# Kernel tuning notes

Hardware: AMD Instinct MI355X
Metric: run time of the kernel (lower is better)

Reference implementation:

```python
import jax, jax.numpy as jnp
import numpy as np

N = 100000
E = 1600000
F_IN, H, C = 128, 128, 64


def setup_inputs() -> dict:
    key = jax.random.key(0)
    ks = jax.random.split(key, 8)
    x = jax.random.normal(ks[0], (N, F_IN), dtype=jnp.float32)
    edge_index = jax.random.randint(ks[1], (2, E), 0, N, dtype=jnp.int64)
    s = lambda fi: (1.0 / np.sqrt(fi))
    # SAGEConv1: lin_l (applied to mean-aggregated neighbors, has bias), lin_r (root, no bias)
    W1l = jax.random.uniform(ks[2], (H, F_IN), jnp.float32, -s(F_IN), s(F_IN))
    b1 = jnp.zeros((H,), jnp.float32)
    W1r = jax.random.uniform(ks[3], (H, F_IN), jnp.float32, -s(F_IN), s(F_IN))
    # SAGEConv2
    W2l = jax.random.uniform(ks[4], (C, H), jnp.float32, -s(H), s(H))
    b2 = jnp.zeros((C,), jnp.float32)
    W2r = jax.random.uniform(ks[5], (C, H), jnp.float32, -s(H), s(H))
    return {"x": x, "edge_index": edge_index, "W1l": W1l, "b1": b1, "W1r": W1r,
            "W2l": W2l, "b2": b2, "W2r": W2r}


def _mean_aggr(x, src, dst):
    # mean over incoming neighbors (PyG flow: edge_index[0]=source -> edge_index[1]=target)
    msg = x[src]                                            # [E, F] big gather
    summed = jax.ops.segment_sum(msg, dst, num_segments=N)  # [N, F]
    cnt = jax.ops.segment_sum(jnp.ones((src.shape[0],), x.dtype), dst, num_segments=N)
    return summed / jnp.clip(cnt, 1.0)[:, None]


def _sage_conv(x, src, dst, Wl, b, Wr):
    agg = _mean_aggr(x, src, dst)
    return agg @ Wl.T + b + x @ Wr.T


def _iconv(x, src, dst):
    # weight-free GCN propagation: D^-1/2 (A + I) D^-1/2 @ x
    loops = jnp.arange(N, dtype=src.dtype)
    s2 = jnp.concatenate([src, loops])
    d2 = jnp.concatenate([dst, loops])
    deg = jax.ops.segment_sum(jnp.ones((s2.shape[0],), x.dtype), d2, num_segments=N)
    dis = jnp.where(deg > 0, jax.lax.rsqrt(jnp.maximum(deg, 1.0)), 0.0)
    norm = dis[s2] * dis[d2]                               # [E+N]
    return jax.ops.segment_sum(norm[:, None] * x[s2], d2, num_segments=N)


def reference(x, edge_index, W1l, b1, W1r, W2l, b2, W2r):
    src, dst = edge_index[0], edge_index[1]
    h = jax.nn.relu(_sage_conv(x, src, dst, W1l, b1, W1r))
    # F.dropout(training=False) -> identity in eval mode
    h = _sage_conv(h, src, dst, W2l, b2, W2r)
    return _iconv(h, src, dst)
```

## Files before the change

### kernel.cpp

```cpp
#include <hip/hip_runtime.h>

#define GN 100000
#define GE 1600000
#define GF 128
#define GH 128
#define GC 64

#define NB 392
#define SLABSZ 5376
#define P1_EDGES 4096

typedef __attribute__((ext_vector_type(8))) short v8s;
typedef __attribute__((ext_vector_type(4))) float v4f;

__device__ __forceinline__ unsigned short f2bf(float f) {
    union { float f; unsigned u; } a; a.f = f;
    unsigned r = a.u + 0x7fff + ((a.u >> 16) & 1);
    return (unsigned short)(r >> 16);
}
__device__ __forceinline__ float bf2f(unsigned short b) {
    union { unsigned u; float f; } a; a.u = ((unsigned)b) << 16;
    return a.f;
}

__global__ __launch_bounds__(256) void bucket_pass1_kernel(
    unsigned* __restrict__ slab, int* __restrict__ bucket_cnt,
    const int* __restrict__ src, const int* __restrict__ dst, int E)
{
    __shared__ int hist[512];
    __shared__ int scanex[512];
    __shared__ int cursor[512];
    __shared__ int gbase[512];
    __shared__ int ssum[256];
    __shared__ unsigned stage[P1_EDGES];
    __shared__ unsigned short sbid[P1_EDGES];

    int tid = threadIdx.x;
    int e0 = blockIdx.x * P1_EDGES;
    int nE = min(P1_EDGES, E - e0);

    unsigned pk[16]; int bk[16];
    hist[tid] = 0; hist[tid + 256] = 0;
    __syncthreads();
    #pragma unroll
    for (int j = 0; j < 16; ++j) {
        int i = j * 256 + tid;
        if (i < nE) {
            int e = e0 + i;
            int d = dst[e], s = src[e];
            int b = d >> 8;
            pk[j] = ((unsigned)(d & 255) << 17) | (unsigned)s;
            bk[j] = b;
            atomicAdd(&hist[b], 1);
        } else bk[j] = -1;
    }
    __syncthreads();
    int a0 = hist[2 * tid], a1 = hist[2 * tid + 1];
    int s2 = a0 + a1;
    ssum[tid] = s2;
    __syncthreads();
    for (int off = 1; off < 256; off <<= 1) {
        int v = (tid >= off) ? ssum[tid - off] : 0;
        __syncthreads();
        ssum[tid] += v;
        __syncthreads();
    }
    int pbase = ssum[tid] - s2;
    scanex[2 * tid] = pbase;          cursor[2 * tid] = pbase;
    scanex[2 * tid + 1] = pbase + a0; cursor[2 * tid + 1] = pbase + a0;
    __syncthreads();
    #pragma unroll
    for (int j = 0; j < 16; ++j) {
        if (bk[j] >= 0) {
            int pos = atomicAdd(&cursor[bk[j]], 1);
            stage[pos] = pk[j];
            sbid[pos] = (unsigned short)bk[j];
        }
    }
    for (int b = tid; b < NB; b += 256) {
        int c = hist[b];
        gbase[b] = c ? atomicAdd(&bucket_cnt[b], c) : 0;
    }
    __syncthreads();
    for (int i = tid; i < nE; i += 256) {
        int b = sbid[i];
        int go = gbase[b] + (i - scanex[b]);
        if (go < SLABSZ)
            slab[(size_t)b * SLABSZ + go] = stage[i];
    }
}

__global__ void bucket_scan_kernel(const int* __restrict__ bucket_cnt,
                                   int* __restrict__ bucket_start,
                                   int* __restrict__ row_ptr, int E) {
    __shared__ int ssum[256];
    int t = threadIdx.x;
    int c0 = (2 * t < NB) ? bucket_cnt[2 * t] : 0;
    int c1 = (2 * t + 1 < NB) ? bucket_cnt[2 * t + 1] : 0;
    int s = c0 + c1;
    ssum[t] = s;
    __syncthreads();
    for (int off = 1; off < 256; off <<= 1) {
        int v = (t >= off) ? ssum[t - off] : 0;
        __syncthreads();
        ssum[t] += v;
        __syncthreads();
    }
    int pbase = ssum[t] - s;
    if (2 * t < NB) bucket_start[2 * t] = pbase;
    if (2 * t + 1 < NB) bucket_start[2 * t + 1] = pbase + c0;
    if (t == 0) row_ptr[GN] = E;
}

__global__ __launch_bounds__(256) void bucket_pass2_kernel(
    int* __restrict__ csr, int* __restrict__ row_ptr,
    float* __restrict__ invc, float* __restrict__ dis,
    const unsigned* __restrict__ slab, const int* __restrict__ bucket_cnt,
    const int* __restrict__ bucket_start)
{
    __shared__ int deg_l[256];
    __shared__ int excl[256];
    __shared__ int cur[256];
    __shared__ int ssum[256];
    __shared__ unsigned stage[SLABSZ];

    int t = threadIdx.x;
    int b = blockIdx.x;
    int cnt = min(bucket_cnt[b], SLABSZ);
    int base = bucket_start[b];
    const unsigned* sp = slab + (size_t)b * SLABSZ;

    deg_l[t] = 0;
    __syncthreads();
    for (int i = t; i < cnt; i += 256)
        atomicAdd(&deg_l[sp[i] >> 17], 1);
    __syncthreads();
    int dg = deg_l[t];
    ssum[t] = dg;
    __syncthreads();
    for (int off = 1; off < 256; off <<= 1) {
        int v = (t >= off) ? ssum[t - off] : 0;
        __syncthreads();
        ssum[t] += v;
        __syncthreads();
    }
    int ex = ssum[t] - dg;
    excl[t] = ex; cur[t] = ex;
    __syncthreads();
    int d = b * 256 + t;
    if (d < GN) {
        row_ptr[d] = base + ex;
        float c = (float)dg;
        invc[d] = 1.0f / fmaxf(c, 1.0f);
        dis[d] = rsqrtf(c + 1.0f);
    }
    for (int i = t; i < cnt; i += 256) {
        unsigned p = sp[i];
        int pos = atomicAdd(&cur[p >> 17], 1);
        stage[pos] = p & 0x1FFFFu;
    }
    __syncthreads();
    for (int i = t; i < cnt; i += 256)
        csr[base + i] = (int)stage[i];
}

__global__ void cast_all_kernel(unsigned short* __restrict__ xb, const float* __restrict__ x,
                                unsigned short* w1l, unsigned short* w1r,
                                unsigned short* w2l, unsigned short* w2r,
                                const float* W1l, const float* W1r,
                                const float* W2l, const float* W2r) {
    int blk = blockIdx.x;
    if (blk < 12500) {
        int i = blk * 256 + threadIdx.x;
        float4 v = ((const float4*)x)[i];
        ushort4 u;
        u.x = f2bf(v.x); u.y = f2bf(v.y); u.z = f2bf(v.z); u.w = f2bf(v.w);
        ((ushort4*)xb)[i] = u;
        return;
    }
    int i = (blk - 12500) * 256 + threadIdx.x;
    const float* s; unsigned short* d; int off;
    if      (i <  4096) { s = W1l; d = w1l; off = i; }
    else if (i <  8192) { s = W1r; d = w1r; off = i - 4096; }
    else if (i < 10240) { s = W2l; d = w2l; off = i - 8192; }
    else if (i < 12288) { s = W2r; d = w2r; off = i - 10240; }
    else return;
    float4 v = ((const float4*)s)[off];
    ushort4 u;
    u.x = f2bf(v.x); u.y = f2bf(v.y); u.z = f2bf(v.z); u.w = f2bf(v.w);
    ((ushort4*)d)[off] = u;
}

__global__ __launch_bounds__(256) void dual_gemm_kernel(
    unsigned short* __restrict__ C,
    const unsigned short* __restrict__ A1, const unsigned short* __restrict__ A2,
    const unsigned short* __restrict__ W1, const unsigned short* __restrict__ W2,
    const float* __restrict__ bias, int M)
{
    int tid = threadIdx.x;
    int wv = tid >> 6, lane = tid & 63;
    int lm = lane & 15, quad = lane >> 4;
    int m_base = blockIdx.x * 256 + wv * 64;
    int n_base = blockIdx.y * 64;

    v4f acc[4][4];
    #pragma unroll
    for (int mt = 0; mt < 4; ++mt)
        #pragma unroll
        for (int nt = 0; nt < 4; ++nt) acc[mt][nt] = (v4f){0.f,0.f,0.f,0.f};

    #pragma unroll
    for (int ks = 0; ks < 4; ++ks) {
        int koff = ks * 32 + quad * 8;
        v8s a1[4], a2[4], b1[4], b2[4];
        #pragma unroll
        for (int mt = 0; mt < 4; ++mt) {
            int row = m_base + mt * 16 + lm;
            if (row < M) {
                a1[mt] = *(const v8s*)(A1 + (size_t)row * 128 + koff);
                a2[mt] = *(const v8s*)(A2 + (size_t)row * 128 + koff);
            } else {
                a1[mt] = (v8s){0,0,0,0,0,0,0,0};
                a2[mt] = (v8s){0,0,0,0,0,0,0,0};
            }
        }
        #pragma unroll
        for (int nt = 0; nt < 4; ++nt) {
            int col = n_base + nt * 16 + lm;
            b1[nt] = *(const v8s*)(W1 + (size_t)col * 128 + koff);
            b2[nt] = *(const v8s*)(W2 + (size_t)col * 128 + koff);
        }
        #pragma unroll
        for (int mt = 0; mt < 4; ++mt)
            #pragma unroll
            for (int nt = 0; nt < 4; ++nt) {
                acc[mt][nt] = __builtin_amdgcn_mfma_f32_16x16x32_bf16(a1[mt], b1[nt], acc[mt][nt], 0, 0, 0);
                acc[mt][nt] = __builtin_amdgcn_mfma_f32_16x16x32_bf16(a2[mt], b2[nt], acc[mt][nt], 0, 0, 0);
            }
    }

    #pragma unroll
    for (int mt = 0; mt < 4; ++mt)
        #pragma unroll
        for (int r = 0; r < 4; ++r) {
            int row = m_base + mt * 16 + quad * 4 + r;
            if (row >= M) continue;
            #pragma unroll
            for (int nt = 0; nt < 4; ++nt) {
                int col = n_base + nt * 16 + lm;
                float v = acc[mt][nt][r] + bias[col];
                v = fmaxf(v, 0.f);
                C[(size_t)row * 128 + col] = f2bf(v);
            }
        }
}

__global__ __launch_bounds__(256) void gemm64_dual_kernel(
    unsigned short* __restrict__ P, unsigned short* __restrict__ Q,
    const unsigned short* __restrict__ A,
    const unsigned short* __restrict__ Wl, const unsigned short* __restrict__ Wr,
    const float* __restrict__ b2, int M)
{
    int tid = threadIdx.x;
    int wv = tid >> 6, lane = tid & 63;
    int lm = lane & 15, quad = lane >> 4;
    int m_base = blockIdx.x * 256 + wv * 64;

    v4f accP[4][4], accQ[4][4];
    #pragma unroll
    for (int mt = 0; mt < 4; ++mt)
        #pragma unroll
        for (int nt = 0; nt < 4; ++nt) {
            accP[mt][nt] = (v4f){0.f,0.f,0.f,0.f};
            accQ[mt][nt] = (v4f){0.f,0.f,0.f,0.f};
        }

    #pragma unroll
    for (int ks = 0; ks < 4; ++ks) {
        int koff = ks * 32 + quad * 8;
        v8s af[4], bl[4], br[4];
        #pragma unroll
        for (int mt = 0; mt < 4; ++mt) {
            int row = m_base + mt * 16 + lm;
            if (row < M) af[mt] = *(const v8s*)(A + (size_t)row * 128 + koff);
            else         af[mt] = (v8s){0,0,0,0,0,0,0,0};
        }
        #pragma unroll
        for (int nt = 0; nt < 4; ++nt) {
            int col = nt * 16 + lm;
            bl[nt] = *(const v8s*)(Wl + (size_t)col * 128 + koff);
            br[nt] = *(const v8s*)(Wr + (size_t)col * 128 + koff);
        }
        #pragma unroll
        for (int mt = 0; mt < 4; ++mt)
            #pragma unroll
            for (int nt = 0; nt < 4; ++nt) {
                accP[mt][nt] = __builtin_amdgcn_mfma_f32_16x16x32_bf16(af[mt], bl[nt], accP[mt][nt], 0, 0, 0);
                accQ[mt][nt] = __builtin_amdgcn_mfma_f32_16x16x32_bf16(af[mt], br[nt], accQ[mt][nt], 0, 0, 0);
            }
    }

    #pragma unroll
    for (int mt = 0; mt < 4; ++mt)
        #pragma unroll
        for (int r = 0; r < 4; ++r) {
            int row = m_base + mt * 16 + quad * 4 + r;
            if (row >= M) continue;
            #pragma unroll
            for (int nt = 0; nt < 4; ++nt) {
                int col = nt * 16 + lm;
                P[(size_t)row * 64 + col] = f2bf(accP[mt][nt][r]);
                Q[(size_t)row * 64 + col] = f2bf(accQ[mt][nt][r] + b2[col]);
            }
        }
}

__global__ __launch_bounds__(256) void gather_mean128_kernel(
    unsigned short* __restrict__ out, const unsigned short* __restrict__ in,
    const float* __restrict__ invc, const int* __restrict__ row_ptr,
    const int* __restrict__ csr, int N)
{
    int wid = (blockIdx.x * 256 + threadIdx.x) >> 6;
    int lane = threadIdx.x & 63;
    if (wid >= N) return;
    int half = lane >> 5, k = lane & 31;
    int beg = row_ptr[wid], end = row_ptr[wid + 1];
    float ax = 0.f, ay = 0.f, az = 0.f, aw = 0.f;
    int j = beg + half;
    for (; j + 6 < end; j += 8) {
        int s0 = csr[j], s1 = csr[j + 2], s2 = csr[j + 4], s3 = csr[j + 6];
        ushort4 a = ((const ushort4*)(in + (size_t)s0 * 128))[k];
        ushort4 b = ((const ushort4*)(in + (size_t)s1 * 128))[k];
        ushort4 c = ((const ushort4*)(in + (size_t)s2 * 128))[k];
        ushort4 d = ((const ushort4*)(in + (size_t)s3 * 128))[k];
        ax += (bf2f(a.x) + bf2f(b.x)) + (bf2f(c.x) + bf2f(d.x));
        ay += (bf2f(a.y) + bf2f(b.y)) + (bf2f(c.y) + bf2f(d.y));
        az += (bf2f(a.z) + bf2f(b.z)) + (bf2f(c.z) + bf2f(d.z));
        aw += (bf2f(a.w) + bf2f(b.w)) + (bf2f(c.w) + bf2f(d.w));
    }
    for (; j < end; j += 2) {
        ushort4 a = ((const ushort4*)(in + (size_t)csr[j] * 128))[k];
        ax += bf2f(a.x); ay += bf2f(a.y); az += bf2f(a.z); aw += bf2f(a.w);
    }
    ax += __shfl_xor(ax, 32); ay += __shfl_xor(ay, 32);
    az += __shfl_xor(az, 32); aw += __shfl_xor(aw, 32);
    if (half == 0) {
        float ic = invc[wid];
        ushort4 o;
        o.x = f2bf(ax * ic); o.y = f2bf(ay * ic);
        o.z = f2bf(az * ic); o.w = f2bf(aw * ic);
        ((ushort4*)(out + (size_t)wid * 128))[k] = o;
    }
}

__global__ __launch_bounds__(256) void gather_combine_kernel(
    unsigned short* __restrict__ h2s, const unsigned short* __restrict__ p,
    const unsigned short* __restrict__ q,
    const float* __restrict__ invc, const float* __restrict__ dis,
    const int* __restrict__ row_ptr, const int* __restrict__ csr, int N)
{
    int wid = (blockIdx.x * 256 + threadIdx.x) >> 6;
    int lane = threadIdx.x & 63;
    if (wid >= N) return;
    int half = lane >> 5, k = lane & 31;
    int beg = row_ptr[wid], end = row_ptr[wid + 1];
    float ax = 0.f, ay = 0.f;
    int j = beg + half;
    for (; j + 6 < end; j += 8) {
        int s0 = csr[j], s1 = csr[j + 2], s2 = csr[j + 4], s3 = csr[j + 6];
        unsigned a = ((const unsigned*)(p + (size_t)s0 * 64))[k];
        unsigned b = ((const unsigned*)(p + (size_t)s1 * 64))[k];
        unsigned c = ((const unsigned*)(p + (size_t)s2 * 64))[k];
        unsigned d = ((const unsigned*)(p + (size_t)s3 * 64))[k];
        ax += (bf2f((unsigned short)(a & 0xffff)) + bf2f((unsigned short)(b & 0xffff)))
            + (bf2f((unsigned short)(c & 0xffff)) + bf2f((unsigned short)(d & 0xffff)));
        ay += (bf2f((unsigned short)(a >> 16)) + bf2f((unsigned short)(b >> 16)))
            + (bf2f((unsigned short)(c >> 16)) + bf2f((unsigned short)(d >> 16)));
    }
    for (; j < end; j += 2) {
        unsigned a = ((const unsigned*)(p + (size_t)csr[j] * 64))[k];
        ax += bf2f((unsigned short)(a & 0xffff));
        ay += bf2f((unsigned short)(a >> 16));
    }
    ax += __shfl_xor(ax, 32); ay += __shfl_xor(ay, 32);
    if (half == 0) {
        float ic = invc[wid], dd = dis[wid];
        unsigned qv = ((const unsigned*)(q + (size_t)wid * 64))[k];
        float ox = dd * (ax * ic + bf2f((unsigned short)(qv & 0xffff)));
        float oy = dd * (ay * ic + bf2f((unsigned short)(qv >> 16)));
        unsigned o = (unsigned)f2bf(ox) | ((unsigned)f2bf(oy) << 16);
        ((unsigned*)(h2s + (size_t)wid * 64))[k] = o;
    }
}

__global__ __launch_bounds__(256) void iconv_kernel(
    float* __restrict__ out, const unsigned short* __restrict__ h2s,
    const float* __restrict__ dis, const int* __restrict__ row_ptr,
    const int* __restrict__ csr, int N)
{
    int wid = (blockIdx.x * 256 + threadIdx.x) >> 6;
    int lane = threadIdx.x & 63;
    if (wid >= N) return;
    int half = lane >> 5, k = lane & 31;
    int beg = row_ptr[wid], end = row_ptr[wid + 1];
    float ax = 0.f, ay = 0.f;
    int j = beg + half;
    for (; j + 6 < end; j += 8) {
        int s0 = csr[j], s1 = csr[j + 2], s2 = csr[j + 4], s3 = csr[j + 6];
        unsigned a = ((const unsigned*)(h2s + (size_t)s0 * 64))[k];
        unsigned b = ((const unsigned*)(h2s + (size_t)s1 * 64))[k];
        unsigned c = ((const unsigned*)(h2s + (size_t)s2 * 64))[k];
        unsigned d = ((const unsigned*)(h2s + (size_t)s3 * 64))[k];
        ax += (bf2f((unsigned short)(a & 0xffff)) + bf2f((unsigned short)(b & 0xffff)))
            + (bf2f((unsigned short)(c & 0xffff)) + bf2f((unsigned short)(d & 0xffff)));
        ay += (bf2f((unsigned short)(a >> 16)) + bf2f((unsigned short)(b >> 16)))
            + (bf2f((unsigned short)(c >> 16)) + bf2f((unsigned short)(d >> 16)));
    }
    for (; j < end; j += 2) {
        unsigned a = ((const unsigned*)(h2s + (size_t)csr[j] * 64))[k];
        ax += bf2f((unsigned short)(a & 0xffff));
        ay += bf2f((unsigned short)(a >> 16));
    }
    ax += __shfl_xor(ax, 32); ay += __shfl_xor(ay, 32);
    if (half == 0) {
        unsigned s = ((const unsigned*)(h2s + (size_t)wid * 64))[k];
        ax += bf2f((unsigned short)(s & 0xffff));
        ay += bf2f((unsigned short)(s >> 16));
        float dd = dis[wid];
        ((float2*)(out + (size_t)wid * 64))[k] = make_float2(dd * ax, dd * ay);
    }
}

extern "C" void kernel_launch(void* const* d_in, const int* in_sizes, int n_in,
                              void* d_out, int out_size, void* d_ws, size_t ws_size,
                              hipStream_t stream) {
    const float* x   = (const float*)d_in[0];
    const int*   ei  = (const int*)d_in[1];
    const float* W1l = (const float*)d_in[2];
    const float* b1  = (const float*)d_in[3];
    const float* W1r = (const float*)d_in[4];
    const float* W2l = (const float*)d_in[5];
    const float* b2  = (const float*)d_in[6];
    const float* W2r = (const float*)d_in[7];
    float* out = (float*)d_out;

    const int* src = ei;
    const int* dst = ei + GE;

    float* invc = (float*)d_ws;
    float* dis  = invc + GN;
    unsigned short* regA = (unsigned short*)(dis + GN);
    unsigned short* regB = regA + (size_t)GN * 128;
    unsigned short* regC = regB + (size_t)GN * 128;
    unsigned short* xb    = regA;
    unsigned short* aggx  = regB;
    unsigned short* hb    = regC;
    unsigned short* pb    = regA;
    unsigned short* qb    = regA + (size_t)GN * 64;
    unsigned short* h2s   = regB;
    unsigned short* w1lb = regC + (size_t)GN * 128;
    unsigned short* w1rb = w1lb + GH * GF;
    unsigned short* w2lb = w1rb + GH * GF;
    unsigned short* w2rb = w2lb + GC * GH;
    int* row_ptr      = (int*)(w2rb + GC * GH);
    int* bucket_cnt   = row_ptr + GN + 1;
    int* bucket_start = bucket_cnt + NB;
    unsigned* slab    = (unsigned*)(bucket_start + NB);
    int* csr          = (int*)(slab + (size_t)NB * SLABSZ);

    const int T = 256;
    const int g_wave = (GN * 64 + T - 1) / T;
    dim3 g_dual((GN + 255) / 256, GH / 64);
    dim3 g_g64((GN + 255) / 256, 1);

    hipMemsetAsync(bucket_cnt, 0, NB * sizeof(int), stream);
    bucket_pass1_kernel<<<(GE + P1_EDGES - 1) / P1_EDGES, T, 0, stream>>>(
        slab, bucket_cnt, src, dst, GE);
    bucket_scan_kernel<<<1, T, 0, stream>>>(bucket_cnt, bucket_start, row_ptr, GE);
    bucket_pass2_kernel<<<NB, T, 0, stream>>>(csr, row_ptr, invc, dis,
                                              slab, bucket_cnt, bucket_start);

    cast_all_kernel<<<12548, T, 0, stream>>>(xb, x, w1lb, w1rb, w2lb, w2rb,
                                             W1l, W1r, W2l, W2r);

    gather_mean128_kernel<<<g_wave, T, 0, stream>>>(aggx, xb, invc, row_ptr, csr, GN);
    dual_gemm_kernel<<<g_dual, T, 0, stream>>>(hb, aggx, xb, w1lb, w1rb, b1, GN);

    gemm64_dual_kernel<<<g_g64, T, 0, stream>>>(pb, qb, hb, w2lb, w2rb, b2, GN);
    gather_combine_kernel<<<g_wave, T, 0, stream>>>(h2s, pb, qb, invc, dis,
                                                    row_ptr, csr, GN);

    iconv_kernel<<<g_wave, T, 0, stream>>>(out, h2s, dis, row_ptr, csr, GN);
}
```

Measured before the change: 396.5 us.

## Fuse bucket pass1 with casts, fold bucket scan into pass2, loop N-halves in GEMM

```diff
diff --git a/kernel.cpp b/kernel.cpp
--- a/kernel.cpp
+++ b/kernel.cpp
@@ -9,6 +9,8 @@
 #define NB 392
 #define SLABSZ 5376
 #define P1_EDGES 4096
+#define P1_BLOCKS ((GE + P1_EDGES - 1) / P1_EDGES)
+#define CASTX_BLOCKS 12500
 
 typedef __attribute__((ext_vector_type(8))) short v8s;
 typedef __attribute__((ext_vector_type(4))) float v4f;
@@ -23,9 +25,14 @@
     return a.f;
 }
 
-__global__ __launch_bounds__(256) void bucket_pass1_kernel(
+__global__ __launch_bounds__(256) void prep_kernel(
     unsigned* __restrict__ slab, int* __restrict__ bucket_cnt,
-    const int* __restrict__ src, const int* __restrict__ dst, int E)
+    const int* __restrict__ src, const int* __restrict__ dst,
+    unsigned short* __restrict__ xb, const float* __restrict__ x,
+    unsigned short* w1l, unsigned short* w1r,
+    unsigned short* w2l, unsigned short* w2r,
+    const float* W1l, const float* W1r,
+    const float* W2l, const float* W2r)
 {
     __shared__ int hist[512];
     __shared__ int scanex[512];
@@ -36,8 +43,34 @@
     __shared__ unsigned short sbid[P1_EDGES];
 
     int tid = threadIdx.x;
-    int e0 = blockIdx.x * P1_EDGES;
-    int nE = min(P1_EDGES, E - e0);
+    int blk = blockIdx.x;
+
+    if (blk >= P1_BLOCKS) {
+        int cb = blk - P1_BLOCKS;
+        if (cb < CASTX_BLOCKS) {
+            int i = cb * 256 + tid;
+            float4 v = ((const float4*)x)[i];
+            ushort4 u;
+            u.x = f2bf(v.x); u.y = f2bf(v.y); u.z = f2bf(v.z); u.w = f2bf(v.w);
+            ((ushort4*)xb)[i] = u;
+            return;
+        }
+        int i = (cb - CASTX_BLOCKS) * 256 + tid;
+        const float* s; unsigned short* d; int off;
+        if      (i <  4096) { s = W1l; d = w1l; off = i; }
+        else if (i <  8192) { s = W1r; d = w1r; off = i - 4096; }
+        else if (i < 10240) { s = W2l; d = w2l; off = i - 8192; }
+        else if (i < 12288) { s = W2r; d = w2r; off = i - 10240; }
+        else return;
+        float4 v = ((const float4*)s)[off];
+        ushort4 u;
+        u.x = f2bf(v.x); u.y = f2bf(v.y); u.z = f2bf(v.z); u.w = f2bf(v.w);
+        ((ushort4*)d)[off] = u;
+        return;
+    }
+
+    int e0 = blk * P1_EDGES;
+    int nE = min(P1_EDGES, GE - e0);
 
     unsigned pk[16]; int bk[16];
     hist[tid] = 0; hist[tid + 256] = 0;
@@ -90,48 +123,42 @@
     }
 }
 
-__global__ void bucket_scan_kernel(const int* __restrict__ bucket_cnt,
-                                   int* __restrict__ bucket_start,
-                                   int* __restrict__ row_ptr, int E) {
-    __shared__ int ssum[256];
-    int t = threadIdx.x;
-    int c0 = (2 * t < NB) ? bucket_cnt[2 * t] : 0;
-    int c1 = (2 * t + 1 < NB) ? bucket_cnt[2 * t + 1] : 0;
-    int s = c0 + c1;
-    ssum[t] = s;
-    __syncthreads();
-    for (int off = 1; off < 256; off <<= 1) {
-        int v = (t >= off) ? ssum[t - off] : 0;
-        __syncthreads();
-        ssum[t] += v;
-        __syncthreads();
-    }
-    int pbase = ssum[t] - s;
-    if (2 * t < NB) bucket_start[2 * t] = pbase;
-    if (2 * t + 1 < NB) bucket_start[2 * t + 1] = pbase + c0;
-    if (t == 0) row_ptr[GN] = E;
-}
-
 __global__ __launch_bounds__(256) void bucket_pass2_kernel(
     int* __restrict__ csr, int* __restrict__ row_ptr,
     float* __restrict__ invc, float* __restrict__ dis,
-    const unsigned* __restrict__ slab, const int* __restrict__ bucket_cnt,
-    const int* __restrict__ bucket_start)
+    const unsigned* __restrict__ slab, const int* __restrict__ bucket_cnt)
 {
     __shared__ int deg_l[256];
     __shared__ int excl[256];
     __shared__ int cur[256];
     __shared__ int ssum[256];
+    __shared__ int bstart_s;
     __shared__ unsigned stage[SLABSZ];
 
     int t = threadIdx.x;
     int b = blockIdx.x;
+
+    int c0 = (2 * t < NB) ? bucket_cnt[2 * t] : 0;
+    int c1 = (2 * t + 1 < NB) ? bucket_cnt[2 * t + 1] : 0;
+    int sc = c0 + c1;
+    ssum[t] = sc;
+    __syncthreads();
+    for (int off = 1; off < 256; off <<= 1) {
+        int v = (t >= off) ? ssum[t - off] : 0;
+        __syncthreads();
+        ssum[t] += v;
+        __syncthreads();
+    }
+    int pb = ssum[t] - sc;
+    if (2 * t == b)     bstart_s = pb;
+    if (2 * t + 1 == b) bstart_s = pb + c0;
+    if (b == NB - 1 && t == 0) row_ptr[GN] = GE;
+
     int cnt = min(bucket_cnt[b], SLABSZ);
-    int base = bucket_start[b];
     const unsigned* sp = slab + (size_t)b * SLABSZ;
-
     deg_l[t] = 0;
     __syncthreads();
+    int base = bstart_s;
     for (int i = t; i < cnt; i += 256)
         atomicAdd(&deg_l[sp[i] >> 17], 1);
     __syncthreads();
@@ -164,33 +191,6 @@
         csr[base + i] = (int)stage[i];
 }
 
-__global__ void cast_all_kernel(unsigned short* __restrict__ xb, const float* __restrict__ x,
-                                unsigned short* w1l, unsigned short* w1r,
-                                unsigned short* w2l, unsigned short* w2r,
-                                const float* W1l, const float* W1r,
-                                const float* W2l, const float* W2r) {
-    int blk = blockIdx.x;
-    if (blk < 12500) {
-        int i = blk * 256 + threadIdx.x;
-        float4 v = ((const float4*)x)[i];
-        ushort4 u;
-        u.x = f2bf(v.x); u.y = f2bf(v.y); u.z = f2bf(v.z); u.w = f2bf(v.w);
-        ((ushort4*)xb)[i] = u;
-        return;
-    }
-    int i = (blk - 12500) * 256 + threadIdx.x;
-    const float* s; unsigned short* d; int off;
-    if      (i <  4096) { s = W1l; d = w1l; off = i; }
-    else if (i <  8192) { s = W1r; d = w1r; off = i - 4096; }
-    else if (i < 10240) { s = W2l; d = w2l; off = i - 8192; }
-    else if (i < 12288) { s = W2r; d = w2r; off = i - 10240; }
-    else return;
-    float4 v = ((const float4*)s)[off];
-    ushort4 u;
-    u.x = f2bf(v.x); u.y = f2bf(v.y); u.z = f2bf(v.z); u.w = f2bf(v.w);
-    ((ushort4*)d)[off] = u;
-}
-
 __global__ __launch_bounds__(256) void dual_gemm_kernel(
     unsigned short* __restrict__ C,
     const unsigned short* __restrict__ A1, const unsigned short* __restrict__ A2,
@@ -201,58 +201,60 @@
     int wv = tid >> 6, lane = tid & 63;
     int lm = lane & 15, quad = lane >> 4;
     int m_base = blockIdx.x * 256 + wv * 64;
-    int n_base = blockIdx.y * 64;
-
-    v4f acc[4][4];
-    #pragma unroll
-    for (int mt = 0; mt < 4; ++mt)
-        #pragma unroll
-        for (int nt = 0; nt < 4; ++nt) acc[mt][nt] = (v4f){0.f,0.f,0.f,0.f};
-
-    #pragma unroll
-    for (int ks = 0; ks < 4; ++ks) {
-        int koff = ks * 32 + quad * 8;
-        v8s a1[4], a2[4], b1[4], b2[4];
-        #pragma unroll
-        for (int mt = 0; mt < 4; ++mt) {
-            int row = m_base + mt * 16 + lm;
-            if (row < M) {
-                a1[mt] = *(const v8s*)(A1 + (size_t)row * 128 + koff);
-                a2[mt] = *(const v8s*)(A2 + (size_t)row * 128 + koff);
-            } else {
-                a1[mt] = (v8s){0,0,0,0,0,0,0,0};
-                a2[mt] = (v8s){0,0,0,0,0,0,0,0};
+
+    for (int nh = 0; nh < 2; ++nh) {
+        int n_base = nh * 64;
+        v4f acc[4][4];
+        #pragma unroll
+        for (int mt = 0; mt < 4; ++mt)
+            #pragma unroll
+            for (int nt = 0; nt < 4; ++nt) acc[mt][nt] = (v4f){0.f,0.f,0.f,0.f};
+
+        #pragma unroll
+        for (int ks = 0; ks < 4; ++ks) {
+            int koff = ks * 32 + quad * 8;
+            v8s a1[4], a2[4], b1[4], b2[4];
+            #pragma unroll
+            for (int mt = 0; mt < 4; ++mt) {
+                int row = m_base + mt * 16 + lm;
+                if (row < M) {
+                    a1[mt] = *(const v8s*)(A1 + (size_t)row * 128 + koff);
+                    a2[mt] = *(const v8s*)(A2 + (size_t)row * 128 + koff);
+                } else {
+                    a1[mt] = (v8s){0,0,0,0,0,0,0,0};
+                    a2[mt] = (v8s){0,0,0,0,0,0,0,0};
+                }
             }
-        }
-        #pragma unroll
-        for (int nt = 0; nt < 4; ++nt) {
-            int col = n_base + nt * 16 + lm;
-            b1[nt] = *(const v8s*)(W1 + (size_t)col * 128 + koff);
-            b2[nt] = *(const v8s*)(W2 + (size_t)col * 128 + koff);
-        }
-        #pragma unroll
-        for (int mt = 0; mt < 4; ++mt)
-            #pragma unroll
-            for (int nt = 0; nt < 4; ++nt) {
-                acc[mt][nt] = __builtin_amdgcn_mfma_f32_16x16x32_bf16(a1[mt], b1[nt], acc[mt][nt], 0, 0, 0);
-                acc[mt][nt] = __builtin_amdgcn_mfma_f32_16x16x32_bf16(a2[mt], b2[nt], acc[mt][nt], 0, 0, 0);
-            }
-    }
-
-    #pragma unroll
-    for (int mt = 0; mt < 4; ++mt)
-        #pragma unroll
-        for (int r = 0; r < 4; ++r) {
-            int row = m_base + mt * 16 + quad * 4 + r;
-            if (row >= M) continue;
             #pragma unroll
             for (int nt = 0; nt < 4; ++nt) {
                 int col = n_base + nt * 16 + lm;
-                float v = acc[mt][nt][r] + bias[col];
-                v = fmaxf(v, 0.f);
-                C[(size_t)row * 128 + col] = f2bf(v);
+                b1[nt] = *(const v8s*)(W1 + (size_t)col * 128 + koff);
+                b2[nt] = *(const v8s*)(W2 + (size_t)col * 128 + koff);
             }
-        }
+            #pragma unroll
+            for (int mt = 0; mt < 4; ++mt)
+                #pragma unroll
+                for (int nt = 0; nt < 4; ++nt) {
+                    acc[mt][nt] = __builtin_amdgcn_mfma_f32_16x16x32_bf16(a1[mt], b1[nt], acc[mt][nt], 0, 0, 0);
+                    acc[mt][nt] = __builtin_amdgcn_mfma_f32_16x16x32_bf16(a2[mt], b2[nt], acc[mt][nt], 0, 0, 0);
+                }
+        }
+
+        #pragma unroll
+        for (int mt = 0; mt < 4; ++mt)
+            #pragma unroll
+            for (int r = 0; r < 4; ++r) {
+                int row = m_base + mt * 16 + quad * 4 + r;
+                if (row >= M) continue;
+                #pragma unroll
+                for (int nt = 0; nt < 4; ++nt) {
+                    int col = n_base + nt * 16 + lm;
+                    float v = acc[mt][nt][r] + bias[col];
+                    v = fmaxf(v, 0.f);
+                    C[(size_t)row * 128 + col] = f2bf(v);
+                }
+            }
+    }
 }
 
 __global__ __launch_bounds__(256) void gemm64_dual_kernel(
@@ -464,24 +466,21 @@
     unsigned short* w2rb = w2lb + GC * GH;
     int* row_ptr      = (int*)(w2rb + GC * GH);
     int* bucket_cnt   = row_ptr + GN + 1;
-    int* bucket_start = bucket_cnt + NB;
-    unsigned* slab    = (unsigned*)(bucket_start + NB);
+    unsigned* slab    = (unsigned*)(bucket_cnt + NB);
     int* csr          = (int*)(slab + (size_t)NB * SLABSZ);
 
     const int T = 256;
     const int g_wave = (GN * 64 + T - 1) / T;
-    dim3 g_dual((GN + 255) / 256, GH / 64);
+    dim3 g_dual((GN + 255) / 256, 1);
     dim3 g_g64((GN + 255) / 256, 1);
 
     hipMemsetAsync(bucket_cnt, 0, NB * sizeof(int), stream);
-    bucket_pass1_kernel<<<(GE + P1_EDGES - 1) / P1_EDGES, T, 0, stream>>>(
-        slab, bucket_cnt, src, dst, GE);
-    bucket_scan_kernel<<<1, T, 0, stream>>>(bucket_cnt, bucket_start, row_ptr, GE);
+    prep_kernel<<<P1_BLOCKS + CASTX_BLOCKS + 48, T, 0, stream>>>(
+        slab, bucket_cnt, src, dst,
+        xb, x, w1lb, w1rb, w2lb, w2rb, W1l, W1r, W2l, W2r);
+
     bucket_pass2_kernel<<<NB, T, 0, stream>>>(csr, row_ptr, invc, dis,
-                                              slab, bucket_cnt, bucket_start);
-
-    cast_all_kernel<<<12548, T, 0, stream>>>(xb, x, w1lb, w1rb, w2lb, w2rb,
-                                             W1l, W1r, W2l, W2r);
+                                              slab, bucket_cnt);
 
     gather_mean128_kernel<<<g_wave, T, 0, stream>>>(aggx, xb, invc, row_ptr, csr, GN);
     dual_gemm_kernel<<<g_dual, T, 0, stream>>>(hb, aggx, xb, w1lb, w1rb, b1, GN);
```

Result: faster. 388.6 us (-2.0%).
